# Performance work log

Measured on AMD Instinct MI355X. Metric: run time of the kernel, lower is better.

Reference implementation:

```python
import jax, jax.numpy as jnp
import numpy as np

B, T, C = 2, 2048, 1024
H, HS = 16, 64
THETA = 10000.0


def _rope_tables(seq_len, dim, dtype):
    inv_freq = 1.0 / (THETA ** (jnp.arange(0, dim, 2, dtype=jnp.float32) / dim))
    t = jnp.arange(seq_len, dtype=jnp.float32)
    freqs = t[:, None] * inv_freq[None, :]          # [T, dim/2]
    emb = jnp.concatenate([freqs, freqs], axis=-1)  # [T, dim]
    return jnp.cos(emb).astype(dtype), jnp.sin(emb).astype(dtype)


def _rotate_half(x):
    x1, x2 = jnp.split(x, 2, axis=-1)
    return jnp.concatenate([-x2, x1], axis=-1)


def setup_inputs() -> dict:
    key = jax.random.key(0)
    ks = jax.random.split(key, 9)
    s = 0.02
    return {
        "q_x": jax.random.normal(ks[0], (B, T, C), dtype=jnp.float32),
        "wq": jax.random.normal(ks[1], (C, H * HS), dtype=jnp.float32) * s,
        "bq": jnp.zeros((H * HS,), dtype=jnp.float32),
        "wk": jax.random.normal(ks[2], (C, H * HS), dtype=jnp.float32) * s,
        "bk": jnp.zeros((H * HS,), dtype=jnp.float32),
        "wv": jax.random.normal(ks[3], (C, H * HS), dtype=jnp.float32) * s,
        "bv": jnp.zeros((H * HS,), dtype=jnp.float32),
        "wc": jax.random.normal(ks[4], (H * HS, C), dtype=jnp.float32) * s,
        "bc": jnp.zeros((C,), dtype=jnp.float32),
    }


def reference(q_x, wq, bq, wk, bk, wv, bv, wc, bc):
    b, t, _ = q_x.shape
    # Q/K/V projections -> [B, H, T, HS]
    q = (q_x @ wq + bq).reshape(b, t, H, HS).transpose(0, 2, 1, 3)
    k = (q_x @ wk + bk).reshape(b, t, H, HS).transpose(0, 2, 1, 3)
    v = (q_x @ wv + bv).reshape(b, t, H, HS).transpose(0, 2, 1, 3)
    # RoPE (concat-half rotation)
    cos, sin = _rope_tables(t, HS, q.dtype)  # [T, HS]
    q = q * cos + _rotate_half(q) * sin
    k = k * cos + _rotate_half(k) * sin
    # Naive causal attention
    scale = 1.0 / np.sqrt(HS)
    att = jnp.einsum("bhqd,bhkd->bhqk", q, k) * scale
    mask = jnp.tril(jnp.ones((t, t), dtype=bool))
    att = jnp.where(mask, att, -jnp.inf)
    att = jax.nn.softmax(att, axis=-1)
    y = jnp.einsum("bhqk,bhkd->bhqd", att, v)
    y = y.transpose(0, 2, 1, 3).reshape(b, t, H * HS)
    return y @ wc + bc
```

## Files before the change

kernel.cpp:

```cpp
#include <hip/hip_runtime.h>

#define B_  2
#define T_  2048
#define C_  1024
#define H_  16
#define HS_ 64
#define M_  4096
#define N_  1024
#define K_  1024

typedef float floatx4 __attribute__((ext_vector_type(4)));
typedef short bf16x8  __attribute__((ext_vector_type(8)));

__device__ __forceinline__ float bf2f(unsigned short u) {
    return __uint_as_float(((unsigned int)u) << 16);
}
__device__ __forceinline__ unsigned short f2bf(float f) {
    unsigned int u = __float_as_uint(f);
    return (unsigned short)((u + 0x7fffu + ((u >> 16) & 1u)) >> 16);
}
__device__ __forceinline__ unsigned int pack2(float a, float b) {
    return (unsigned int)f2bf(a) | ((unsigned int)f2bf(b) << 16);
}
__device__ __forceinline__ unsigned int pack2t(float a, float b) {
    return __builtin_amdgcn_perm(__float_as_uint(b), __float_as_uint(a), 0x07060302u);
}
__device__ __forceinline__ void async16(const unsigned short* g, unsigned short* l) {
    __builtin_amdgcn_global_load_lds(
        (const __attribute__((address_space(1))) unsigned int*)g,
        (__attribute__((address_space(3))) unsigned int*)l, 16, 0, 0);
}

__global__ __launch_bounds__(256) void prep_kernel(
    const float* __restrict__ x,
    const float* __restrict__ w0, const float* __restrict__ w1,
    const float* __restrict__ w2, const float* __restrict__ w3,
    unsigned short* __restrict__ xb, unsigned short* __restrict__ wTall)
{
    __shared__ float tile[64][65];
    const int bid = blockIdx.x;
    const int t = threadIdx.x;
    if (bid < 4096) {
        const size_t i = ((size_t)bid * 256 + t) * 4;
        const float4 v = *(const float4*)(x + i);
        ushort4 st;
        st.x = f2bf(v.x); st.y = f2bf(v.y); st.z = f2bf(v.z); st.w = f2bf(v.w);
        *(ushort4*)(xb + i) = st;
        return;
    }
    const int zb = bid - 4096;
    const int z = zb >> 8, rem = zb & 255;
    const float* w = (z == 0) ? w0 : (z == 1) ? w1 : (z == 2) ? w2 : w3;
    unsigned short* wT = wTall + ((size_t)z << 20);
    const int n0 = (rem & 15) * 64, k0 = (rem >> 4) * 64;

    const int r = t >> 2, cq = (t & 3) * 16;
    const float4* src = (const float4*)(w + (size_t)(k0 + r) * N_ + n0 + cq);
    const float4 v0 = src[0], v1 = src[1], v2 = src[2], v3 = src[3];
    tile[r][cq+0]=v0.x; tile[r][cq+1]=v0.y; tile[r][cq+2]=v0.z; tile[r][cq+3]=v0.w;
    tile[r][cq+4]=v1.x; tile[r][cq+5]=v1.y; tile[r][cq+6]=v1.z; tile[r][cq+7]=v1.w;
    tile[r][cq+8]=v2.x; tile[r][cq+9]=v2.y; tile[r][cq+10]=v2.z; tile[r][cq+11]=v2.w;
    tile[r][cq+12]=v3.x; tile[r][cq+13]=v3.y; tile[r][cq+14]=v3.z; tile[r][cq+15]=v3.w;
    __syncthreads();

    const int rn = t >> 2, ck = (t & 3) * 16;
    unsigned int o[8];
#pragma unroll
    for (int ii = 0; ii < 8; ii++)
        o[ii] = pack2(tile[ck + 2*ii][rn], tile[ck + 2*ii + 1][rn]);
    unsigned short* dst = wT + (size_t)(n0 + rn) * K_ + k0 + ck;
    *(uint4*)dst       = make_uint4(o[0], o[1], o[2], o[3]);
    *(uint4*)(dst + 8) = make_uint4(o[4], o[5], o[6], o[7]);
}

__global__ __launch_bounds__(256) void qkv_gemm(
    const unsigned short* __restrict__ xb, const unsigned short* __restrict__ wT,
    const float* __restrict__ bq, const float* __restrict__ bk,
    const float* __restrict__ bv,
    unsigned short* __restrict__ qb, unsigned short* __restrict__ kb,
    unsigned short* __restrict__ vb)
{
    __shared__ unsigned short As[2 * 128 * 32];
    __shared__ unsigned short Bs[2 * 128 * 32];

    const int tid  = threadIdx.x;
    const int lane = tid & 63;
    const int wave = tid >> 6;
    const int p  = blockIdx.x >> 3;
    const int n0 = (blockIdx.x & 7) * 128;
    const int m0 = blockIdx.y * 128;
    const float* bias = (p == 0) ? bq : (p == 1) ? bk : bv;

    const int lrow = lane >> 2, lch = (lane & 3) * 8;
    const unsigned short* ag0 = xb + (size_t)(m0 + wave * 32 + lrow) * K_ + lch;
    const unsigned short* ag1 = ag0 + (size_t)16 * K_;
    const unsigned short* wb  = wT + ((size_t)p << 20);
    const unsigned short* bg0 = wb + (size_t)(n0 + wave * 32 + lrow) * K_ + lch;
    const unsigned short* bg1 = bg0 + (size_t)16 * K_;
    unsigned short* lA00 = &As[(wave * 32) * 32];
    unsigned short* lA01 = &As[(wave * 32 + 16) * 32];
    unsigned short* lA10 = lA00 + 4096;
    unsigned short* lA11 = lA01 + 4096;
    unsigned short* lB00 = &Bs[(wave * 32) * 32];
    unsigned short* lB01 = &Bs[(wave * 32 + 16) * 32];
    unsigned short* lB10 = lB00 + 4096;
    unsigned short* lB11 = lB01 + 4096;

    const int fr = lane & 15;
    const int fk = (lane >> 4) * 8;
    const int wr = wave >> 1, wc = wave & 1;

    floatx4 acc[4][4];
#pragma unroll
    for (int i = 0; i < 4; i++)
#pragma unroll
        for (int j = 0; j < 4; j++) acc[i][j] = (floatx4){0.f, 0.f, 0.f, 0.f};

    for (int k0 = 0; k0 < K_; k0 += 64) {
        __syncthreads();
        async16(ag0 + k0,      lA00);
        async16(ag1 + k0,      lA01);
        async16(ag0 + k0 + 32, lA10);
        async16(ag1 + k0 + 32, lA11);
        async16(bg0 + k0,      lB00);
        async16(bg1 + k0,      lB01);
        async16(bg0 + k0 + 32, lB10);
        async16(bg1 + k0 + 32, lB11);
        __syncthreads();

#pragma unroll
        for (int kh = 0; kh < 2; kh++) {
            const unsigned short* Ah = &As[kh * 4096];
            const unsigned short* Bh = &Bs[kh * 4096];
            bf16x8 af[4], bfr[4];
#pragma unroll
            for (int i = 0; i < 4; i++)
                af[i] = *(const bf16x8*)&Ah[(wr * 64 + i * 16 + fr) * 32 + fk];
#pragma unroll
            for (int j = 0; j < 4; j++)
                bfr[j] = *(const bf16x8*)&Bh[(wc * 64 + j * 16 + fr) * 32 + fk];
#pragma unroll
            for (int i = 0; i < 4; i++)
#pragma unroll
                for (int j = 0; j < 4; j++)
                    acc[i][j] = __builtin_amdgcn_mfma_f32_16x16x32_bf16(
                        af[i], bfr[j], acc[i][j], 0, 0, 0);
        }
    }

    const int rbase = (lane >> 4) * 4;
    const int h = (n0 + wc * 64) >> 6;
    if (p == 2) {
#pragma unroll
        for (int j = 0; j < 4; j++) {
            const int col = n0 + wc * 64 + j * 16 + fr;
            const float bz = bias[col];
            const int d = col & 63;
#pragma unroll
            for (int i = 0; i < 4; i++) {
                const int row0 = m0 + wr * 64 + i * 16 + rbase;
                const int bb = row0 >> 11, tt = row0 & 2047;
                ushort4 st;
                st.x = f2bf(acc[i][j][0] + bz);
                st.y = f2bf(acc[i][j][1] + bz);
                st.z = f2bf(acc[i][j][2] + bz);
                st.w = f2bf(acc[i][j][3] + bz);
                *(ushort4*)&vb[((size_t)(bb * H_ + h) * HS_ + d) * T_ + tt] = st;
            }
        }
    } else {
        unsigned short* out = (p == 0) ? qb : kb;
        const float qsc = (p == 0) ? 0.18033688011111772f : 1.0f;
        const float bz0 = bias[n0 + wc * 64 + fr];
        const float bz1 = bias[n0 + wc * 64 + 16 + fr];
        const float bz2 = bias[n0 + wc * 64 + 32 + fr];
        const float bz3 = bias[n0 + wc * 64 + 48 + fr];
        const float nl = -0.41524101186279297f;
        const float if0 = exp2f((float)fr * nl);
        const float if1 = exp2f((float)(fr + 16) * nl);
#pragma unroll
        for (int i = 0; i < 4; i++) {
#pragma unroll
            for (int pr = 0; pr < 4; pr++) {
                const int row = m0 + wr * 64 + i * 16 + rbase + pr;
                const int bb = row >> 11, tt = row & 2047;
                float s0, c0, s1, c1;
                __sincosf((float)tt * if0, &s0, &c0);
                __sincosf((float)tt * if1, &s1, &c1);
                const float v0 = acc[i][0][pr] + bz0;
                const float v1 = acc[i][1][pr] + bz1;
                const float v2 = acc[i][2][pr] + bz2;
                const float v3 = acc[i][3][pr] + bz3;
                unsigned short* ob = out + ((size_t)(bb * H_ + h) * T_ + tt) * HS_ + fr;
                ob[0]  = f2bf((v0 * c0 - v2 * s0) * qsc);
                ob[16] = f2bf((v1 * c1 - v3 * s1) * qsc);
                ob[32] = f2bf((v2 * c0 + v0 * s0) * qsc);
                ob[48] = f2bf((v3 * c1 + v1 * s1) * qsc);
            }
        }
    }
}

__global__ __launch_bounds__(256) void attn_kernel(
    const unsigned short* __restrict__ qb, const unsigned short* __restrict__ kb,
    const unsigned short* __restrict__ vt, unsigned short* __restrict__ yb,
    unsigned short* __restrict__ Opart, float* __restrict__ Mpart)
{
    __shared__ unsigned short Ks[2][64 * 64];
    __shared__ unsigned short Vs[2][64 * 64];
    __shared__ unsigned short Ps[4][16 * 64];

    const int bh = blockIdx.x;
    const int b = bh >> 4, h = bh & 15;
    const int s = 47 - (int)blockIdx.y;
    int qt, ktlo, kthi, half;
    bool split;
    if (s < 16) { qt = s; ktlo = 0; kthi = qt; half = 0; split = false; }
    else {
        const int idx = s - 16;
        qt = 16 + (idx >> 1); half = idx & 1;
        const int nf = (qt + 2) >> 1;
        ktlo = half ? nf : 0;
        kthi = half ? qt : nf - 1;
        split = true;
    }
    const int r0 = qt * 64;
    const int tid  = threadIdx.x;
    const int lane = tid & 63;
    const int wave = tid >> 6;
    const int l4   = lane & 15;
    const int quad = lane >> 4;

    const int qrow_g = r0 + wave * 16 + l4;

    bf16x8 qf[2];
    {
        const unsigned short* qp = qb + ((size_t)bh * T_ + qrow_g) * HS_ + quad * 8;
        qf[0] = *(const bf16x8*)(qp);
        qf[1] = *(const bf16x8*)(qp + 32);
    }

    floatx4 o[4];
#pragma unroll
    for (int g = 0; g < 4; g++) o[g] = (floatx4){0.f, 0.f, 0.f, 0.f};
    float m = -1e30f, l = 0.f;

    const int srow = tid >> 2;
    const int sc16 = (tid & 3) * 16;
    const int ssw  = (srow & 7) * 8;
    const int psw  = (l4 & 7) * 8;

    const unsigned short* kp = kb + ((size_t)bh * T_ + srow) * HS_ + sc16;
    const unsigned short* vp = vt + ((size_t)(bh * 64 + srow)) * T_ + sc16;

    uint4 rk0 = *(const uint4*)(kp + (size_t)ktlo * 64 * HS_);
    uint4 rk1 = *(const uint4*)(kp + (size_t)ktlo * 64 * HS_ + 8);
    uint4 rv0 = *(const uint4*)(vp + ktlo * 64);
    uint4 rv1 = *(const uint4*)(vp + ktlo * 64 + 8);
    *(uint4*)&Ks[0][srow * 64 + ( sc16      ^ ssw)] = rk0;
    *(uint4*)&Ks[0][srow * 64 + ((sc16 + 8) ^ ssw)] = rk1;
    *(uint4*)&Vs[0][srow * 64 + ( sc16      ^ ssw)] = rv0;
    *(uint4*)&Vs[0][srow * 64 + ((sc16 + 8) ^ ssw)] = rv1;

    for (int kt = ktlo; kt <= kthi; kt++) {
        const int cur = (kt - ktlo) & 1;
        if (kt < kthi) {
            const unsigned short* kpn = kp + (size_t)(kt + 1) * (64 * HS_);
            const unsigned short* vpn = vp + (kt + 1) * 64;
            rk0 = *(const uint4*)kpn;
            rk1 = *(const uint4*)(kpn + 8);
            rv0 = *(const uint4*)vpn;
            rv1 = *(const uint4*)(vpn + 8);
        }
        __syncthreads();

        floatx4 sf[4];
#pragma unroll
        for (int mg = 0; mg < 4; mg++) {
            const int key = mg * 16 + l4;
            const int ksw = (key & 7) * 8;
            const bf16x8 a0 = *(const bf16x8*)&Ks[cur][key * 64 + ( (quad * 8)       ^ ksw)];
            const bf16x8 a1 = *(const bf16x8*)&Ks[cur][key * 64 + (((quad * 8) + 32) ^ ksw)];
            floatx4 z = (floatx4){0.f, 0.f, 0.f, 0.f};
            z = __builtin_amdgcn_mfma_f32_16x16x32_bf16(a0, qf[0], z, 0, 0, 0);
            z = __builtin_amdgcn_mfma_f32_16x16x32_bf16(a1, qf[1], z, 0, 0, 0);
            sf[mg] = z;
        }

        if (kt == qt) {
#pragma unroll
            for (int mg = 0; mg < 4; mg++)
#pragma unroll
                for (int r = 0; r < 4; r++)
                    if (kt * 64 + 16 * mg + quad * 4 + r > qrow_g)
                        sf[mg][r] = -1e30f;
        }

        float tm = sf[0][0];
#pragma unroll
        for (int mg = 0; mg < 4; mg++)
#pragma unroll
            for (int r = 0; r < 4; r++) tm = fmaxf(tm, sf[mg][r]);
        tm = fmaxf(tm, __shfl_xor(tm, 16));
        tm = fmaxf(tm, __shfl_xor(tm, 32));
        const float mnew  = fmaxf(m, tm);
        const float alpha = __builtin_amdgcn_exp2f(m - mnew);

        float p[4][4];
        float ps = 0.f;
#pragma unroll
        for (int mg = 0; mg < 4; mg++)
#pragma unroll
            for (int r = 0; r < 4; r++) {
                p[mg][r] = __builtin_amdgcn_exp2f(sf[mg][r] - mnew);
                ps += p[mg][r];
            }
        ps += __shfl_xor(ps, 16);
        ps += __shfl_xor(ps, 32);
        l = l * alpha + ps;
        m = mnew;
#pragma unroll
        for (int g = 0; g < 4; g++) o[g] = o[g] * alpha;

#pragma unroll
        for (int mg = 0; mg < 4; mg++) {
            const int kb4 = 16 * mg + quad * 4;
            const int off = ((kb4 & ~7) ^ psw) | (kb4 & 7);
            uint2 w;
            w.x = pack2t(p[mg][0], p[mg][1]);
            w.y = pack2t(p[mg][2], p[mg][3]);
            *(uint2*)&Ps[wave][l4 * 64 + off] = w;
        }

        const bf16x8 pf0 = *(const bf16x8*)&Ps[wave][l4 * 64 + ( (quad * 8)       ^ psw)];
        const bf16x8 pf1 = *(const bf16x8*)&Ps[wave][l4 * 64 + (((quad * 8) + 32) ^ psw)];
#pragma unroll
        for (int g = 0; g < 4; g++) {
            const int vd  = g * 16 + l4;
            const int vsw = (vd & 7) * 8;
            const bf16x8 va0 = *(const bf16x8*)&Vs[cur][vd * 64 + ( (quad * 8)       ^ vsw)];
            const bf16x8 va1 = *(const bf16x8*)&Vs[cur][vd * 64 + (((quad * 8) + 32) ^ vsw)];
            o[g] = __builtin_amdgcn_mfma_f32_16x16x32_bf16(va0, pf0, o[g], 0, 0, 0);
            o[g] = __builtin_amdgcn_mfma_f32_16x16x32_bf16(va1, pf1, o[g], 0, 0, 0);
        }

        if (kt < kthi) {
            const int nxt = cur ^ 1;
            *(uint4*)&Ks[nxt][srow * 64 + ( sc16      ^ ssw)] = rk0;
            *(uint4*)&Ks[nxt][srow * 64 + ((sc16 + 8) ^ ssw)] = rk1;
            *(uint4*)&Vs[nxt][srow * 64 + ( sc16      ^ ssw)] = rv0;
            *(uint4*)&Vs[nxt][srow * 64 + ((sc16 + 8) ^ ssw)] = rv1;
        }
    }

    if (!split) {
        const float invl = 1.f / l;
        unsigned short* yrow = yb + ((size_t)(b * T_ + qrow_g) * H_ + h) * HS_;
#pragma unroll
        for (int g = 0; g < 4; g++) {
            ushort4 st;
            st.x = f2bf(o[g][0] * invl);
            st.y = f2bf(o[g][1] * invl);
            st.z = f2bf(o[g][2] * invl);
            st.w = f2bf(o[g][3] * invl);
            *(ushort4*)&yrow[16 * g + quad * 4] = st;
        }
    } else {
        const int u  = (bh * 16 + (qt - 16)) * 2 + half;
        const int rl = wave * 16 + l4;
        unsigned short* Op = Opart + (size_t)u * 4096 + rl * 64;
#pragma unroll
        for (int g = 0; g < 4; g++) {
            ushort4 st;
            st.x = f2bf(o[g][0]);
            st.y = f2bf(o[g][1]);
            st.z = f2bf(o[g][2]);
            st.w = f2bf(o[g][3]);
            *(ushort4*)&Op[16 * g + quad * 4] = st;
        }
        if (quad == 0) {
            float* ml = Mpart + (size_t)u * 128;
            ml[rl]      = m;
            ml[64 + rl] = l;
        }
    }
}

__global__ __launch_bounds__(256) void attn_combine(
    const unsigned short* __restrict__ Opart, const float* __restrict__ Mpart,
    unsigned short* __restrict__ yb)
{
    const int u  = blockIdx.x;
    const int bh = u >> 4, qt = 16 + (u & 15);
    const int b = bh >> 4, h = bh & 15;
    const int t = threadIdx.x;
    const int r = t >> 2, c = (t & 3) * 16;

    const float* ml1 = Mpart + (size_t)(u * 2) * 128;
    const float* ml2 = ml1 + 128;
    const float m1 = ml1[r], l1 = ml1[64 + r];
    const float m2 = ml2[r], l2 = ml2[64 + r];
    const float M  = fmaxf(m1, m2);
    const float w1 = __builtin_amdgcn_exp2f(m1 - M);
    const float w2 = __builtin_amdgcn_exp2f(m2 - M);
    const float inv = 1.f / (l1 * w1 + l2 * w2);
    const float a1 = w1 * inv, a2 = w2 * inv;

    const unsigned short* O1 = Opart + (size_t)(u * 2)     * 4096 + r * 64 + c;
    const unsigned short* O2 = Opart + (size_t)(u * 2 + 1) * 4096 + r * 64 + c;
    unsigned short* yrow = yb + ((size_t)(b * T_ + qt * 64 + r) * H_ + h) * HS_ + c;

#pragma unroll
    for (int j = 0; j < 2; j++) {
        const uint4 u1 = *(const uint4*)(O1 + 8 * j);
        const uint4 u2 = *(const uint4*)(O2 + 8 * j);
        const unsigned int a[4] = {u1.x, u1.y, u1.z, u1.w};
        const unsigned int d[4] = {u2.x, u2.y, u2.z, u2.w};
        unsigned int ov[4];
#pragma unroll
        for (int q = 0; q < 4; q++) {
            const float y0 = bf2f((unsigned short)(a[q] & 0xffff)) * a1
                           + bf2f((unsigned short)(d[q] & 0xffff)) * a2;
            const float y1 = bf2f((unsigned short)(a[q] >> 16)) * a1
                           + bf2f((unsigned short)(d[q] >> 16)) * a2;
            ov[q] = pack2(y0, y1);
        }
        *(uint4*)(yrow + 8 * j) = make_uint4(ov[0], ov[1], ov[2], ov[3]);
    }
}

__global__ __launch_bounds__(256) void out_gemm(
    const unsigned short* __restrict__ A, const unsigned short* __restrict__ wcT,
    const float* __restrict__ bias, float* __restrict__ out)
{
    __shared__ unsigned short As[2 * 64 * 32];
    __shared__ unsigned short Bs[2 * 128 * 32];

    const int tid  = threadIdx.x;
    const int lane = tid & 63;
    const int wave = tid >> 6;
    const int n0 = blockIdx.x * 128;
    const int m0 = blockIdx.y * 64;

    const int lrow = lane >> 2, lch = (lane & 3) * 8;
    const unsigned short* ag  = A   + (size_t)(m0 + wave * 16 + lrow) * K_ + lch;
    const unsigned short* bg0 = wcT + (size_t)(n0 + wave * 32 + lrow) * K_ + lch;
    const unsigned short* bg1 = bg0 + (size_t)16 * K_;
    unsigned short* lA0  = &As[(wave * 16) * 32];
    unsigned short* lA1  = lA0 + 2048;
    unsigned short* lB00 = &Bs[(wave * 32) * 32];
    unsigned short* lB01 = &Bs[(wave * 32 + 16) * 32];
    unsigned short* lB10 = lB00 + 4096;
    unsigned short* lB11 = lB01 + 4096;

    const int fr = lane & 15;
    const int fk = (lane >> 4) * 8;
    const int wr2 = wave >> 1, wc2 = wave & 1;

    floatx4 acc[2][4];
#pragma unroll
    for (int i = 0; i < 2; i++)
#pragma unroll
        for (int j = 0; j < 4; j++) acc[i][j] = (floatx4){0.f, 0.f, 0.f, 0.f};

    for (int k0 = 0; k0 < K_; k0 += 64) {
        __syncthreads();
        async16(ag  + k0,      lA0);
        async16(ag  + k0 + 32, lA1);
        async16(bg0 + k0,      lB00);
        async16(bg1 + k0,      lB01);
        async16(bg0 + k0 + 32, lB10);
        async16(bg1 + k0 + 32, lB11);
        __syncthreads();

#pragma unroll
        for (int kh = 0; kh < 2; kh++) {
            const unsigned short* Ah = &As[kh * 2048];
            const unsigned short* Bh = &Bs[kh * 4096];
            bf16x8 af[2], bfr[4];
#pragma unroll
            for (int i = 0; i < 2; i++)
                af[i] = *(const bf16x8*)&Ah[(wr2 * 32 + i * 16 + fr) * 32 + fk];
#pragma unroll
            for (int j = 0; j < 4; j++)
                bfr[j] = *(const bf16x8*)&Bh[(wc2 * 64 + j * 16 + fr) * 32 + fk];
#pragma unroll
            for (int i = 0; i < 2; i++)
#pragma unroll
                for (int j = 0; j < 4; j++)
                    acc[i][j] = __builtin_amdgcn_mfma_f32_16x16x32_bf16(
                        af[i], bfr[j], acc[i][j], 0, 0, 0);
        }
    }

    const int rbase = (lane >> 4) * 4;
#pragma unroll
    for (int j = 0; j < 4; j++) {
        const int col = n0 + wc2 * 64 + j * 16 + fr;
        const float bz = bias[col];
#pragma unroll
        for (int i = 0; i < 2; i++) {
#pragma unroll
            for (int pr = 0; pr < 4; pr++) {
                const int row = m0 + wr2 * 32 + i * 16 + rbase + pr;
                out[(size_t)row * N_ + col] = acc[i][j][pr] + bz;
            }
        }
    }
}

extern "C" void kernel_launch(void* const* d_in, const int* in_sizes, int n_in,
                              void* d_out, int out_size, void* d_ws, size_t ws_size,
                              hipStream_t stream) {
    const float* x  = (const float*)d_in[0];
    const float* wq = (const float*)d_in[1];
    const float* bq = (const float*)d_in[2];
    const float* wk = (const float*)d_in[3];
    const float* bk = (const float*)d_in[4];
    const float* wv = (const float*)d_in[5];
    const float* bv = (const float*)d_in[6];
    const float* wc = (const float*)d_in[7];
    const float* bc = (const float*)d_in[8];
    float* out = (float*)d_out;

    unsigned short* ws  = (unsigned short*)d_ws;
    unsigned short* qb  = ws;
    unsigned short* kb  = ws + (size_t)4194304;
    unsigned short* vb  = ws + (size_t)8388608;
    unsigned short* yb  = ws + (size_t)12582912;
    unsigned short* xb  = ws + (size_t)16777216;
    unsigned short* wT  = ws + (size_t)20971520;
    unsigned short* wcT = wT + ((size_t)3 << 20);
    unsigned short* Opart = xb;
    float*          Mpart = (float*)wT;

    prep_kernel<<<5120, 256, 0, stream>>>(x, wq, wk, wv, wc, xb, wT);
    qkv_gemm<<<dim3(24, 32), 256, 0, stream>>>(xb, wT, bq, bk, bv, qb, kb, vb);
    attn_kernel<<<dim3(32, 48), 256, 0, stream>>>(qb, kb, vb, yb, Opart, Mpart);
    attn_combine<<<512, 256, 0, stream>>>(Opart, Mpart, yb);
    out_gemm<<<dim3(8, 64), 256, 0, stream>>>(yb, wcT, bc, out);
}
```

Measured before the change: 195.0 us.

## Rewrite QKV GEMM with 256x256 tiles, double-buffered swizzled LDS and ping-pong schedule

Rewrites the QKV projection GEMM to use 512-thread blocks computing 256x256 output tiles over a flat 192-block grid with an XCD-aware block swizzle. Global-to-LDS async loads are double-buffered and issued in quarter stages interleaved with MFMA phases. The schedule uses explicit barriers, waitcnts and setprio around the MFMA clusters, and LDS rows are XOR-swizzled to avoid bank conflicts. This aims to hide memory latency and raise MFMA utilisation. In exchange it uses 128KB of LDS and many accumulator registers, and 192 blocks may leave some CUs idle.

```diff
diff --git a/kernel.cpp b/kernel.cpp
--- a/kernel.cpp
+++ b/kernel.cpp
@@ -73,92 +73,167 @@
     *(uint4*)(dst + 8) = make_uint4(o[4], o[5], o[6], o[7]);
 }
 
-__global__ __launch_bounds__(256) void qkv_gemm(
+__global__ __launch_bounds__(512, 2) void qkv_gemm(
     const unsigned short* __restrict__ xb, const unsigned short* __restrict__ wT,
     const float* __restrict__ bq, const float* __restrict__ bk,
     const float* __restrict__ bv,
     unsigned short* __restrict__ qb, unsigned short* __restrict__ kb,
     unsigned short* __restrict__ vb)
 {
-    __shared__ unsigned short As[2 * 128 * 32];
-    __shared__ unsigned short Bs[2 * 128 * 32];
+    __shared__ unsigned short lds[65536];
 
     const int tid  = threadIdx.x;
     const int lane = tid & 63;
     const int wave = tid >> 6;
-    const int p  = blockIdx.x >> 3;
-    const int n0 = (blockIdx.x & 7) * 128;
-    const int m0 = blockIdx.y * 128;
+
+    const int bid = blockIdx.x;
+    const int swz = (bid & 7) * 24 + (bid >> 3);
+    const int nb  = swz % 12;
+    const int mb  = swz / 12;
+    const int m0  = mb * 256;
+    const int n0g = nb * 256;
+
+    const int wm = wave >> 2, wn = wave & 3;
+    const int fr = lane & 15, quad = lane >> 4;
+
+    const int r_s = tid >> 2;
+    const int c_s = (tid & 3) ^ ((tid >> 3) & 3);
+    const unsigned short* aS0 = xb + (size_t)(m0 + r_s) * 1024 + c_s * 8;
+    const unsigned short* aS1 = aS0 + (size_t)128 * 1024;
+    const unsigned short* bS0 = wT + (size_t)(n0g + r_s) * 1024 + c_s * 8;
+    const unsigned short* bS1 = bS0 + (size_t)128 * 1024;
+    unsigned short* ldw = &lds[wave * 512];
+
+    auto stage = [&](int buf, int region, const unsigned short* s0,
+                     const unsigned short* s1) {
+        unsigned short* d = ldw + buf * 32768 + region * 8192;
+        async16(s0, d);
+        async16(s1, d + 4096);
+    };
+
+    int oA[8], oB[4];
+#pragma unroll
+    for (int i = 0; i < 8; i++) {
+        const int r = wm * 128 + i * 16 + fr;
+        oA[i] = r * 32 + ((quad ^ ((r >> 1) & 3)) << 3);
+    }
+#pragma unroll
+    for (int j = 0; j < 4; j++) {
+        const int r = wn * 64 + j * 16 + fr;
+        oB[j] = r * 32 + ((quad ^ ((r >> 1) & 3)) << 3);
+    }
+
+    floatx4 acc[8][4];
+#pragma unroll
+    for (int i = 0; i < 8; i++)
+#pragma unroll
+        for (int j = 0; j < 4; j++) acc[i][j] = (floatx4){0.f, 0.f, 0.f, 0.f};
+
+    stage(0, 0, aS0,      aS1);
+    stage(0, 2, bS0,      bS1);
+    stage(0, 1, aS0 + 32, aS1 + 32);
+    stage(0, 3, bS0 + 32, bS1 + 32);
+    stage(1, 0, aS0 + 64, aS1 + 64);
+    stage(1, 2, bS0 + 64, bS1 + 64);
+    asm volatile("s_waitcnt vmcnt(8)" ::: "memory");
+    __builtin_amdgcn_s_barrier();
+    __builtin_amdgcn_sched_barrier(0);
+
+    bf16x8 af[4], bfr[4];
+#pragma unroll 2
+    for (int t = 0; t < 16; ++t) {
+        const int cur = t & 1, nxt = cur ^ 1;
+        const unsigned short* A0 = &lds[cur * 32768];
+        const unsigned short* A1 = A0 + 8192;
+        const unsigned short* B0 = A0 + 16384;
+        const unsigned short* B1 = A0 + 24576;
+        const int k1 = (t + 1) * 64, k2 = (t + 2) * 64;
+
+#pragma unroll
+        for (int i = 0; i < 4; i++) af[i]  = *(const bf16x8*)&A0[oA[i]];
+#pragma unroll
+        for (int j = 0; j < 4; j++) bfr[j] = *(const bf16x8*)&B0[oB[j]];
+        if (t + 1 < 16) stage(nxt, 1, aS0 + k1 + 32, aS1 + k1 + 32);
+        __builtin_amdgcn_s_barrier();
+        asm volatile("s_waitcnt lgkmcnt(0)" ::: "memory");
+        __builtin_amdgcn_s_setprio(1);
+#pragma unroll
+        for (int i = 0; i < 4; i++)
+#pragma unroll
+            for (int j = 0; j < 4; j++)
+                acc[i][j] = __builtin_amdgcn_mfma_f32_16x16x32_bf16(
+                    af[i], bfr[j], acc[i][j], 0, 0, 0);
+        __builtin_amdgcn_s_setprio(0);
+        __builtin_amdgcn_s_barrier();
+        __builtin_amdgcn_sched_barrier(0);
+
+#pragma unroll
+        for (int i = 0; i < 4; i++) af[i] = *(const bf16x8*)&A0[oA[4 + i]];
+        if (t + 1 < 16) stage(nxt, 3, bS0 + k1 + 32, bS1 + k1 + 32);
+        asm volatile("s_waitcnt vmcnt(8)" ::: "memory");
+        __builtin_amdgcn_s_barrier();
+        asm volatile("s_waitcnt lgkmcnt(0)" ::: "memory");
+        __builtin_amdgcn_s_setprio(1);
+#pragma unroll
+        for (int i = 0; i < 4; i++)
+#pragma unroll
+            for (int j = 0; j < 4; j++)
+                acc[4 + i][j] = __builtin_amdgcn_mfma_f32_16x16x32_bf16(
+                    af[i], bfr[j], acc[4 + i][j], 0, 0, 0);
+        __builtin_amdgcn_s_setprio(0);
+        __builtin_amdgcn_s_barrier();
+        __builtin_amdgcn_sched_barrier(0);
+
+#pragma unroll
+        for (int i = 0; i < 4; i++) af[i]  = *(const bf16x8*)&A1[oA[i]];
+#pragma unroll
+        for (int j = 0; j < 4; j++) bfr[j] = *(const bf16x8*)&B1[oB[j]];
+        if (t + 2 < 16) stage(cur, 0, aS0 + k2, aS1 + k2);
+        __builtin_amdgcn_s_barrier();
+        asm volatile("s_waitcnt lgkmcnt(0)" ::: "memory");
+        __builtin_amdgcn_s_setprio(1);
+#pragma unroll
+        for (int i = 0; i < 4; i++)
+#pragma unroll
+            for (int j = 0; j < 4; j++)
+                acc[i][j] = __builtin_amdgcn_mfma_f32_16x16x32_bf16(
+                    af[i], bfr[j], acc[i][j], 0, 0, 0);
+        __builtin_amdgcn_s_setprio(0);
+        __builtin_amdgcn_s_barrier();
+        __builtin_amdgcn_sched_barrier(0);
+
+#pragma unroll
+        for (int i = 0; i < 4; i++) af[i] = *(const bf16x8*)&A1[oA[4 + i]];
+        if (t + 2 < 16) stage(cur, 2, bS0 + k2, bS1 + k2);
+        asm volatile("s_waitcnt vmcnt(8)" ::: "memory");
+        __builtin_amdgcn_s_barrier();
+        asm volatile("s_waitcnt lgkmcnt(0)" ::: "memory");
+        __builtin_amdgcn_s_setprio(1);
+#pragma unroll
+        for (int i = 0; i < 4; i++)
+#pragma unroll
+            for (int j = 0; j < 4; j++)
+                acc[4 + i][j] = __builtin_amdgcn_mfma_f32_16x16x32_bf16(
+                    af[i], bfr[j], acc[4 + i][j], 0, 0, 0);
+        __builtin_amdgcn_s_setprio(0);
+        __builtin_amdgcn_s_barrier();
+        __builtin_amdgcn_sched_barrier(0);
+    }
+
+    const int p = nb >> 2;
+    const int colbase = (nb & 3) * 256 + wn * 64;
+    const int h = colbase >> 6;
+    const int rb = quad * 4;
     const float* bias = (p == 0) ? bq : (p == 1) ? bk : bv;
 
-    const int lrow = lane >> 2, lch = (lane & 3) * 8;
-    const unsigned short* ag0 = xb + (size_t)(m0 + wave * 32 + lrow) * K_ + lch;
-    const unsigned short* ag1 = ag0 + (size_t)16 * K_;
-    const unsigned short* wb  = wT + ((size_t)p << 20);
-    const unsigned short* bg0 = wb + (size_t)(n0 + wave * 32 + lrow) * K_ + lch;
-    const unsigned short* bg1 = bg0 + (size_t)16 * K_;
-    unsigned short* lA00 = &As[(wave * 32) * 32];
-    unsigned short* lA01 = &As[(wave * 32 + 16) * 32];
-    unsigned short* lA10 = lA00 + 4096;
-    unsigned short* lA11 = lA01 + 4096;
-    unsigned short* lB00 = &Bs[(wave * 32) * 32];
-    unsigned short* lB01 = &Bs[(wave * 32 + 16) * 32];
-    unsigned short* lB10 = lB00 + 4096;
-    unsigned short* lB11 = lB01 + 4096;
-
-    const int fr = lane & 15;
-    const int fk = (lane >> 4) * 8;
-    const int wr = wave >> 1, wc = wave & 1;
-
-    floatx4 acc[4][4];
-#pragma unroll
-    for (int i = 0; i < 4; i++)
-#pragma unroll
-        for (int j = 0; j < 4; j++) acc[i][j] = (floatx4){0.f, 0.f, 0.f, 0.f};
-
-    for (int k0 = 0; k0 < K_; k0 += 64) {
-        __syncthreads();
-        async16(ag0 + k0,      lA00);
-        async16(ag1 + k0,      lA01);
-        async16(ag0 + k0 + 32, lA10);
-        async16(ag1 + k0 + 32, lA11);
-        async16(bg0 + k0,      lB00);
-        async16(bg1 + k0,      lB01);
-        async16(bg0 + k0 + 32, lB10);
-        async16(bg1 + k0 + 32, lB11);
-        __syncthreads();
-
-#pragma unroll
-        for (int kh = 0; kh < 2; kh++) {
-            const unsigned short* Ah = &As[kh * 4096];
-            const unsigned short* Bh = &Bs[kh * 4096];
-            bf16x8 af[4], bfr[4];
-#pragma unroll
-            for (int i = 0; i < 4; i++)
-                af[i] = *(const bf16x8*)&Ah[(wr * 64 + i * 16 + fr) * 32 + fk];
-#pragma unroll
-            for (int j = 0; j < 4; j++)
-                bfr[j] = *(const bf16x8*)&Bh[(wc * 64 + j * 16 + fr) * 32 + fk];
-#pragma unroll
-            for (int i = 0; i < 4; i++)
-#pragma unroll
-                for (int j = 0; j < 4; j++)
-                    acc[i][j] = __builtin_amdgcn_mfma_f32_16x16x32_bf16(
-                        af[i], bfr[j], acc[i][j], 0, 0, 0);
-        }
-    }
-
-    const int rbase = (lane >> 4) * 4;
-    const int h = (n0 + wc * 64) >> 6;
     if (p == 2) {
 #pragma unroll
         for (int j = 0; j < 4; j++) {
-            const int col = n0 + wc * 64 + j * 16 + fr;
-            const float bz = bias[col];
-            const int d = col & 63;
-#pragma unroll
-            for (int i = 0; i < 4; i++) {
-                const int row0 = m0 + wr * 64 + i * 16 + rbase;
+            const int d = j * 16 + fr;
+            const float bz = bias[colbase + d];
+#pragma unroll
+            for (int i = 0; i < 8; i++) {
+                const int row0 = m0 + wm * 128 + i * 16 + rb;
                 const int bb = row0 >> 11, tt = row0 & 2047;
                 ushort4 st;
                 st.x = f2bf(acc[i][j][0] + bz);
@@ -171,18 +246,18 @@
     } else {
         unsigned short* out = (p == 0) ? qb : kb;
         const float qsc = (p == 0) ? 0.18033688011111772f : 1.0f;
-        const float bz0 = bias[n0 + wc * 64 + fr];
-        const float bz1 = bias[n0 + wc * 64 + 16 + fr];
-        const float bz2 = bias[n0 + wc * 64 + 32 + fr];
-        const float bz3 = bias[n0 + wc * 64 + 48 + fr];
+        const float bz0 = bias[colbase + fr];
+        const float bz1 = bias[colbase + 16 + fr];
+        const float bz2 = bias[colbase + 32 + fr];
+        const float bz3 = bias[colbase + 48 + fr];
         const float nl = -0.41524101186279297f;
         const float if0 = exp2f((float)fr * nl);
         const float if1 = exp2f((float)(fr + 16) * nl);
 #pragma unroll
-        for (int i = 0; i < 4; i++) {
+        for (int i = 0; i < 8; i++) {
 #pragma unroll
             for (int pr = 0; pr < 4; pr++) {
-                const int row = m0 + wr * 64 + i * 16 + rbase + pr;
+                const int row = m0 + wm * 128 + i * 16 + rb + pr;
                 const int bb = row >> 11, tt = row & 2047;
                 float s0, c0, s1, c1;
                 __sincosf((float)tt * if0, &s0, &c0);
@@ -535,7 +610,7 @@
     float*          Mpart = (float*)wT;
 
     prep_kernel<<<5120, 256, 0, stream>>>(x, wq, wk, wv, wc, xb, wT);
-    qkv_gemm<<<dim3(24, 32), 256, 0, stream>>>(xb, wT, bq, bk, bv, qb, kb, vb);
+    qkv_gemm<<<192, 512, 0, stream>>>(xb, wT, bq, bk, bv, qb, kb, vb);
     attn_kernel<<<dim3(32, 48), 256, 0, stream>>>(qb, kb, vb, yb, Opart, Mpart);
     attn_combine<<<512, 256, 0, stream>>>(Opart, Mpart, yb);
     out_gemm<<<dim3(8, 64), 256, 0, stream>>>(yb, wcT, bc, out);
```

Result: faster. 188.1 us (-3.5%).
